# Kernel optimization log

Hardware: AMD Instinct MI355X
Metric: run time of the kernel (lower is better)

## Reference

```python
import jax, jax.numpy as jnp
import numpy as np

NEG_INF = -1e30  # stand-in for -inf in additive causal mask (softmax-safe)


def rotary_pos_emb(x):
    # x: [B, T, H, D]. Faithful to source: freqs = 1/1000**(arange(0,D,2)//D)
    # with INTEGER floor division -> exponent 0 -> all freqs == 1.0.
    B, T, H, D = x.shape
    exponents = (jnp.arange(0, D, 2)[: D // 2] // D).astype(jnp.float32)
    freqs = 1.0 / jnp.power(jnp.float32(1000.0), exponents)          # [D/2]
    theta = jnp.arange(T, dtype=jnp.float32)[:, None] * freqs[None, :]  # [T, D/2]
    cos = jnp.cos(theta)[None, :, None, :]  # [1, T, 1, D/2]
    sin = jnp.sin(theta)[None, :, None, :]
    xr = x.astype(jnp.float32).reshape(B, T, H, D // 2, 2)
    x0, x1 = xr[..., 0], xr[..., 1]
    # complex multiply (x0 + i x1) * (cos + i sin)
    out = jnp.stack([x0 * cos - x1 * sin, x0 * sin + x1 * cos], axis=-1)
    return out.reshape(B, T, H, D).astype(x.dtype)


def attention_fwd(x, wq, wk, wv, wo, n_heads=32):
    B, T, C = x.shape
    hd = C // n_heads  # head_dim = 128
    # nn.Linear(bias=False): y = x @ W^T with W: [out, in]
    xq = (x @ wq.T).reshape(B, T, n_heads, hd)
    xk = (x @ wk.T).reshape(B, T, n_heads, hd)
    xv = (x @ wv.T).reshape(B, T, n_heads, hd)
    xq = rotary_pos_emb(xq)
    xk = rotary_pos_emb(xk)
    # n_rep == 1 -> repeat_kv is identity
    scale = hd ** -0.5
    scores = jnp.einsum('bqhd,bkhd->bhqk', xq, xk) * scale  # [B,H,T,T]
    causal = jnp.tril(jnp.ones((T, T), dtype=bool))
    scores = jnp.where(causal[None, None], scores, NEG_INF)
    probs = jax.nn.softmax(scores.astype(jnp.float32), axis=-1).astype(xq.dtype)
    out = jnp.einsum('bhqk,bkhd->bqhd', probs, xv).reshape(B, T, C)
    return out @ wo.T


def setup_inputs() -> dict:
    key = jax.random.key(0)
    ks = jax.random.split(key, 5)
    B, T, C = 2, 2048, 4096
    s = 0.02
    return {
        'x': jax.random.normal(ks[0], (B, T, C), jnp.float32),
        'wq': jax.random.normal(ks[1], (C, C), jnp.float32) * s,
        'wk': jax.random.normal(ks[2], (C, C), jnp.float32) * s,
        'wv': jax.random.normal(ks[3], (C, C), jnp.float32) * s,
        'wo': jax.random.normal(ks[4], (C, C), jnp.float32) * s,
    }


def reference(x, wq, wk, wv, wo):
    return attention_fwd(x, wq, wk, wv, wo)
```

## Files before the change

### kernel.cpp

```cpp
#include <hip/hip_runtime.h>
#include <hip/hip_bf16.h>
#include <stdint.h>

typedef __bf16 bf16_t;
typedef __attribute__((ext_vector_type(8))) __bf16 bf16x8;
typedef __attribute__((ext_vector_type(4))) float f32x4;

#define GLL16(gptr, lptr)                                                      \
  __builtin_amdgcn_global_load_lds(                                            \
      (__attribute__((address_space(1))) void*)(gptr),                         \
      (__attribute__((address_space(3))) void*)(lptr), 16, 0, 0)

__global__ __launch_bounds__(256) void cast5_kernel(const float* __restrict__ x,
                                                    const float* __restrict__ wq,
                                                    const float* __restrict__ wk,
                                                    const float* __restrict__ wv,
                                                    const float* __restrict__ wo,
                                                    bf16_t* __restrict__ outbase) {
  const size_t SZ = (size_t)4096 * 4096;
  const float* in;
  switch (blockIdx.y) {
    case 0: in = x; break;
    case 1: in = wq; break;
    case 2: in = wk; break;
    case 3: in = wv; break;
    default: in = wo; break;
  }
  bf16_t* out = outbase + (size_t)blockIdx.y * SZ;
  int i = blockIdx.x * 256 + threadIdx.x;
  const float4* p = (const float4*)in + (size_t)i * 2;
  float4 a = p[0], b = p[1];
  bf16x8 o;
  o[0] = (__bf16)a.x; o[1] = (__bf16)a.y; o[2] = (__bf16)a.z; o[3] = (__bf16)a.w;
  o[4] = (__bf16)b.x; o[5] = (__bf16)b.y; o[6] = (__bf16)b.z; o[7] = (__bf16)b.w;
  *((bf16x8*)out + i) = o;
}

#define STAGE_HALF(gbase, ldsbase)                                             \
  do {                                                                         \
    GLL16((gbase) + (size_t)(w * 32 + sr) * 4096 + sq, (ldsbase) + w * 1024);  \
    GLL16((gbase) + (size_t)(w * 32 + 16 + sr) * 4096 + sq,                    \
          (ldsbase) + w * 1024 + 512);                                         \
  } while (0)

#define HALF(buf_, kk_, S1_, S2_, TAIL_)                                       \
  do {                                                                         \
    bf16x8 af0_[4], af1_[4];                                                   \
    _Pragma("unroll") for (int ni = 0; ni < 4; ++ni) bfr[ni] =                 \
        *(const bf16x8*)&Bs[buf_][kk_][(wc * 64 + ni * 16 + l15) * 32 + sl8];  \
    _Pragma("unroll") for (int mi = 0; mi < 4; ++mi) af0_[mi] =                \
        *(const bf16x8*)&As[buf_][kk_][(wr * 128 + mi * 16 + l15) * 32 + sl8]; \
    S1_;                                                                       \
    __builtin_amdgcn_sched_barrier(0);                                         \
    _Pragma("unroll") for (int mi = 0; mi < 4; ++mi) af1_[mi] =                \
        *(const bf16x8*)&As[buf_][kk_][(wr * 128 + 64 + mi * 16 + l15) * 32 +  \
                                       sl8];                                   \
    asm volatile("s_waitcnt lgkmcnt(4)" ::: "memory");                         \
    __builtin_amdgcn_sched_barrier(0);                                         \
    __builtin_amdgcn_s_setprio(1);                                             \
    _Pragma("unroll") for (int mi = 0; mi < 4; ++mi)                           \
        _Pragma("unroll") for (int ni = 0; ni < 4; ++ni)                       \
            acc[mi][ni] = __builtin_amdgcn_mfma_f32_16x16x32_bf16(             \
                af0_[mi], bfr[ni], acc[mi][ni], 0, 0, 0);                      \
    __builtin_amdgcn_s_setprio(0);                                             \
    S2_;                                                                       \
    asm volatile("s_waitcnt lgkmcnt(0)" ::: "memory");                         \
    __builtin_amdgcn_sched_barrier(0);                                         \
    __builtin_amdgcn_s_setprio(1);                                             \
    _Pragma("unroll") for (int mi = 0; mi < 4; ++mi)                           \
        _Pragma("unroll") for (int ni = 0; ni < 4; ++ni)                       \
            acc[4 + mi][ni] = __builtin_amdgcn_mfma_f32_16x16x32_bf16(         \
                af1_[mi], bfr[ni], acc[4 + mi][ni], 0, 0, 0);                  \
    __builtin_amdgcn_s_setprio(0);                                             \
    TAIL_;                                                                     \
    __builtin_amdgcn_s_barrier();                                              \
  } while (0)

#define GEMM256_MAIN(Aptr, Bptr)                                               \
  const bf16_t* Ag = (Aptr) + (size_t)bm * 4096;                               \
  const bf16_t* Bg = (Bptr) + (size_t)bn * 4096;                               \
  f32x4 acc[8][4] = {};                                                        \
  bf16x8 bfr[4];                                                               \
  STAGE_HALF(Ag, &As[0][0][0]);                                                \
  STAGE_HALF(Bg, &Bs[0][0][0]);                                                \
  STAGE_HALF(Ag + 32, &As[0][1][0]);                                           \
  STAGE_HALF(Bg + 32, &Bs[0][1][0]);                                           \
  STAGE_HALF(Ag + 64, &As[1][0][0]);                                           \
  STAGE_HALF(Bg + 64, &Bs[1][0][0]);                                           \
  asm volatile("s_waitcnt vmcnt(4)" ::: "memory");                             \
  __builtin_amdgcn_s_barrier();                                                \
  for (int it = 0; it < 32; ++it) {                                            \
    const int kt = it * 2;                                                     \
    const bool more = (it < 31);                                               \
                                                    \
    HALF(0, 0,                                                                 \
         STAGE_HALF(Ag + (size_t)(kt + 1) * 64 + 32, &As[1][1][0]),            \
         STAGE_HALF(Bg + (size_t)(kt + 1) * 64 + 32, &Bs[1][1][0]), (void)0);  \
    HALF(0, 1,                                                                 \
         if (more) STAGE_HALF(Ag + (size_t)(kt + 2) * 64, &As[0][0][0]),       \
         if (more) STAGE_HALF(Bg + (size_t)(kt + 2) * 64, &Bs[0][0][0]),       \
         if (more) { asm volatile("s_waitcnt vmcnt(4)" ::: "memory"); } else { \
           asm volatile("s_waitcnt vmcnt(0)" ::: "memory"); });                \
                                                  \
    HALF(1, 0,                                                                 \
         if (more) STAGE_HALF(Ag + (size_t)(kt + 2) * 64 + 32, &As[0][1][0]),  \
         if (more) STAGE_HALF(Bg + (size_t)(kt + 2) * 64 + 32, &Bs[0][1][0]),  \
         (void)0);                                                             \
    HALF(1, 1,                                                                 \
         if (more) STAGE_HALF(Ag + (size_t)(kt + 3) * 64, &As[1][0][0]),       \
         if (more) STAGE_HALF(Bg + (size_t)(kt + 3) * 64, &Bs[1][0][0]),       \
         if (more) { asm volatile("s_waitcnt vmcnt(4)" ::: "memory"); });      \
  }

__device__ __forceinline__ void epi_rope256(const f32x4 (&acc)[8][4],
                                            bf16_t* __restrict__ C, int bm,
                                            int bn, int wr, int wc, int quad,
                                            int l15) {
#pragma unroll
  for (int a = 0; a < 8; ++a) {
    const int row0 = bm + wr * 128 + a * 16 + quad * 4;
    float fsv[4], fcv[4];
#pragma unroll
    for (int r = 0; r < 4; ++r)
      sincosf((float)((row0 + r) & 2047), &fsv[r], &fcv[r]);
#pragma unroll
    for (int ni = 0; ni < 4; ++ni) {
      const int col = bn + wc * 64 + ni * 16 + l15;
      const bool odd = (col & 1);
#pragma unroll
      for (int r = 0; r < 4; ++r) {
        float v = acc[a][ni][r];
        float pr = __shfl_xor(v, 1, 64);
        float o = odd ? (pr * fsv[r] + v * fcv[r]) : (v * fcv[r] - pr * fsv[r]);
        C[(size_t)(row0 + r) * 4096 + col] = (__bf16)o;
      }
    }
  }
}

__device__ __forceinline__ void epi_vt256(const f32x4 (&acc)[8][4],
                                          bf16_t* __restrict__ VT, int bm,
                                          int bn, int wr, int wc, int quad,
                                          int l15) {
#pragma unroll
  for (int a = 0; a < 8; ++a) {
    const int row0 = bm + wr * 128 + a * 16 + quad * 4;
    const int b = row0 >> 11, t0 = row0 & 2047;
#pragma unroll
    for (int ni = 0; ni < 4; ++ni) {
      const int col = bn + wc * 64 + ni * 16 + l15;
      const int h = col >> 7, d = col & 127;
      union { __bf16 e[4]; uint2 u; } pk;
#pragma unroll
      for (int r = 0; r < 4; ++r) pk.e[r] = (__bf16)acc[a][ni][r];
      *(uint2*)&VT[((size_t)((b * 32 + h) * 128 + d)) * 2048 + t0] = pk.u;
    }
  }
}

__global__ __launch_bounds__(512, 2) void gemm_qkv(const bf16_t* __restrict__ X,
                                                   const bf16_t* __restrict__ WQ,
                                                   const bf16_t* __restrict__ WK,
                                                   const bf16_t* __restrict__ WV,
                                                   bf16_t* __restrict__ Qo,
                                                   bf16_t* __restrict__ Ko,
                                                   bf16_t* __restrict__ VTo) {
  __shared__ bf16_t As[2][2][8192];
  __shared__ bf16_t Bs[2][2][8192];
  const int tid = threadIdx.x;
  const int w = tid >> 6;
  const int lane = tid & 63;
  const int quad = lane >> 4;
  const int l15 = lane & 15;
  const int wr = w >> 2, wc = w & 3;
  const int sr = lane >> 2;
  const int sq = (((lane & 3) ^ ((lane >> 3) & 3))) * 8;
  const int sl8 = (quad ^ ((l15 >> 1) & 3)) * 8;
  const int mat = blockIdx.y;
  int id = blockIdx.x;
  id = (id & 7) * 32 + (id >> 3);
  const int bm = (id >> 4) * 256, bn = (id & 15) * 256;
  const bf16_t* Bp = (mat == 0) ? WQ : (mat == 1) ? WK : WV;

  GEMM256_MAIN(X, Bp)

  if (mat == 0)
    epi_rope256(acc, Qo, bm, bn, wr, wc, quad, l15);
  else if (mat == 1)
    epi_rope256(acc, Ko, bm, bn, wr, wc, quad, l15);
  else
    epi_vt256(acc, VTo, bm, bn, wr, wc, quad, l15);
}

__global__ __launch_bounds__(512, 2) void gemm_out(const bf16_t* __restrict__ A,
                                                   const bf16_t* __restrict__ B,
                                                   float* __restrict__ C) {
  __shared__ bf16_t As[2][2][8192];
  __shared__ bf16_t Bs[2][2][8192];
  const int tid = threadIdx.x;
  const int w = tid >> 6;
  const int lane = tid & 63;
  const int quad = lane >> 4;
  const int l15 = lane & 15;
  const int wr = w >> 2, wc = w & 3;
  const int sr = lane >> 2;
  const int sq = (((lane & 3) ^ ((lane >> 3) & 3))) * 8;
  const int sl8 = (quad ^ ((l15 >> 1) & 3)) * 8;
  int id = blockIdx.x;
  id = (id & 7) * 32 + (id >> 3);
  const int bm = (id >> 4) * 256, bn = (id & 15) * 256;

  GEMM256_MAIN(A, B)

#pragma unroll
  for (int a = 0; a < 8; ++a) {
    const int row0 = bm + wr * 128 + a * 16 + quad * 4;
#pragma unroll
    for (int ni = 0; ni < 4; ++ni) {
      const int col = bn + wc * 64 + ni * 16 + l15;
#pragma unroll
      for (int r = 0; r < 4; ++r)
        C[(size_t)(row0 + r) * 4096 + col] = acc[a][ni][r];
    }
  }
}

__global__ __launch_bounds__(256) void attn_kernel(const bf16_t* __restrict__ Q,
                                                   const bf16_t* __restrict__ Km,
                                                   const bf16_t* __restrict__ VT,
                                                   bf16_t* __restrict__ O) {
  __shared__ bf16_t Ks[64 * 128];
  __shared__ bf16_t Vts[128 * 64];
  __shared__ bf16_t QPs[64 * 128];
  const int tid = threadIdx.x;
  const int w = tid >> 6;
  const int lane = tid & 63;
  const int quad = lane >> 4;
  const int l15 = lane & 15;
  const int bh = blockIdx.x;
  const int qtile = 31 - blockIdx.y;
  const int mrow_base = (bh >> 5) * 2048;
  const int h = bh & 31;
  const float scale = 0.08838834764831845f;

#pragma unroll
  for (int it = 0; it < 4; ++it) {
    int c = w * 4 + it;
    int row = c * 4 + (lane >> 4);
    int cc = (lane & 15) ^ (row & 15);
    GLL16(Q + (size_t)(mrow_base + qtile * 64 + row) * 4096 + h * 128 + cc * 8,
          &QPs[c * 512]);
  }
  __syncthreads();
  bf16x8 qf[4];
#pragma unroll
  for (int ks = 0; ks < 4; ++ks) {
    int row = w * 16 + l15;
    int slot = (ks * 4 + quad) ^ (row & 15);
    qf[ks] = *(const bf16x8*)&QPs[row * 128 + slot * 8];
  }
  bf16_t* Pw = &QPs[w * 16 * 72];

  f32x4 accO[8] = {};
  float mrun[4], lrun[4];
#pragma unroll
  for (int r = 0; r < 4; ++r) { mrun[r] = -1e30f; lrun[r] = 0.f; }

  for (int kt = 0; kt <= qtile; ++kt) {
    __syncthreads();
#pragma unroll
    for (int it = 0; it < 4; ++it) {
      int c = w * 4 + it;
      int krow = c * 4 + (lane >> 4);
      int kcc = (lane & 15) ^ (krow & 15);
      GLL16(Km + (size_t)(mrow_base + kt * 64 + krow) * 4096 + h * 128 + kcc * 8,
            &Ks[c * 512]);
      int vrow = c * 8 + (lane >> 3);
      int vcc = (lane & 7) ^ (vrow & 7);
      GLL16(VT + (size_t)(bh * 128 + vrow) * 2048 + kt * 64 + vcc * 8,
            &Vts[c * 512]);
    }
    __syncthreads();

    f32x4 s[4];
#pragma unroll
    for (int ni = 0; ni < 4; ++ni) {
      s[ni] = (f32x4){0.f, 0.f, 0.f, 0.f};
#pragma unroll
      for (int ks = 0; ks < 4; ++ks) {
        int row = ni * 16 + l15;
        int slot = (ks * 4 + quad) ^ (row & 15);
        bf16x8 kf = *(const bf16x8*)&Ks[row * 128 + slot * 8];
        s[ni] = __builtin_amdgcn_mfma_f32_16x16x32_bf16(qf[ks], kf, s[ni], 0, 0, 0);
      }
    }
    const bool diag = (kt == qtile);
#pragma unroll
    for (int ni = 0; ni < 4; ++ni)
#pragma unroll
      for (int r = 0; r < 4; ++r) {
        float v = s[ni][r] * scale;
        if (diag && (ni * 16 + l15) > (w * 16 + quad * 4 + r)) v = -1e30f;
        s[ni][r] = v;
      }
    float mx[4], alpha[4], rs[4];
#pragma unroll
    for (int r = 0; r < 4; ++r)
      mx[r] = fmaxf(fmaxf(s[0][r], s[1][r]), fmaxf(s[2][r], s[3][r]));
#pragma unroll
    for (int off = 1; off < 16; off <<= 1)
#pragma unroll
      for (int r = 0; r < 4; ++r) mx[r] = fmaxf(mx[r], __shfl_xor(mx[r], off, 64));
    float ps[4][4];
#pragma unroll
    for (int r = 0; r < 4; ++r) {
      float mn = fmaxf(mrun[r], mx[r]);
      alpha[r] = __expf(mrun[r] - mn);
      mrun[r] = mn;
      rs[r] = 0.f;
    }
#pragma unroll
    for (int ni = 0; ni < 4; ++ni)
#pragma unroll
      for (int r = 0; r < 4; ++r) {
        float p = __expf(s[ni][r] - mrun[r]);
        ps[ni][r] = p;
        rs[r] += p;
      }
#pragma unroll
    for (int off = 1; off < 16; off <<= 1)
#pragma unroll
      for (int r = 0; r < 4; ++r) rs[r] += __shfl_xor(rs[r], off, 64);
#pragma unroll
    for (int r = 0; r < 4; ++r) lrun[r] = lrun[r] * alpha[r] + rs[r];
#pragma unroll
    for (int nt = 0; nt < 8; ++nt)
#pragma unroll
      for (int r = 0; r < 4; ++r) accO[nt][r] *= alpha[r];
#pragma unroll
    for (int ni = 0; ni < 4; ++ni)
#pragma unroll
      for (int r = 0; r < 4; ++r)
        Pw[(quad * 4 + r) * 72 + ni * 16 + l15] = (__bf16)ps[ni][r];
    asm volatile("s_waitcnt lgkmcnt(0)" ::: "memory");
    bf16x8 pf[2];
#pragma unroll
    for (int ks = 0; ks < 2; ++ks)
      pf[ks] = *(const bf16x8*)&Pw[l15 * 72 + ks * 32 + quad * 8];
#pragma unroll
    for (int nt = 0; nt < 8; ++nt)
#pragma unroll
      for (int ks = 0; ks < 2; ++ks) {
        int vrow = nt * 16 + l15;
        int slot = (ks * 4 + quad) ^ (vrow & 7);
        bf16x8 vf = *(const bf16x8*)&Vts[vrow * 64 + slot * 8];
        accO[nt] = __builtin_amdgcn_mfma_f32_16x16x32_bf16(pf[ks], vf, accO[nt], 0, 0, 0);
      }
  }

#pragma unroll
  for (int r = 0; r < 4; ++r) lrun[r] = 1.f / lrun[r];
#pragma unroll
  for (int nt = 0; nt < 8; ++nt)
#pragma unroll
    for (int r = 0; r < 4; ++r) {
      int trow = qtile * 64 + w * 16 + quad * 4 + r;
      int d = nt * 16 + l15;
      O[(size_t)(mrow_base + trow) * 4096 + h * 128 + d] =
          (__bf16)(accO[nt][r] * lrun[r]);
    }
}

extern "C" void kernel_launch(void* const* d_in, const int* in_sizes, int n_in,
                              void* d_out, int out_size, void* d_ws, size_t ws_size,
                              hipStream_t stream) {
  (void)in_sizes; (void)n_in; (void)out_size; (void)ws_size;
  const float* x = (const float*)d_in[0];
  const float* wq = (const float*)d_in[1];
  const float* wk = (const float*)d_in[2];
  const float* wv = (const float*)d_in[3];
  const float* wo = (const float*)d_in[4];
  float* out = (float*)d_out;

  const size_t SZ = (size_t)4096 * 4096;
  bf16_t* xb = (bf16_t*)d_ws;
  bf16_t* wqb = xb + SZ;
  bf16_t* wkb = wqb + SZ;
  bf16_t* wvb = wkb + SZ;
  bf16_t* wob = wvb + SZ;
  bf16_t* qb = wob + SZ;
  bf16_t* kb = qb + SZ;
  bf16_t* vtb = kb + SZ;
  bf16_t* ab = vtb + SZ;

  dim3 b256(256), b512(512);
  cast5_kernel<<<dim3((unsigned)(SZ / 8 / 256), 5), b256, 0, stream>>>(
      x, wq, wk, wv, wo, xb);

  gemm_qkv<<<dim3(256, 3), b512, 0, stream>>>(xb, wqb, wkb, wvb, qb, kb, vtb);

  attn_kernel<<<dim3(64, 32), b256, 0, stream>>>(qb, kb, vtb, ab);

  gemm_out<<<dim3(256), b512, 0, stream>>>(ab, wob, out);
}
```

Baseline: 1.009 ms.

## Double-buffer K/V tiles in attention kernel to overlap loads with MFMA

Splits the attention kernel's K and V shared-memory tiles into two buffers. The next key tile is prefetched with global_load_lds while the current one is being computed, so global-memory latency overlaps with the MFMA and softmax work. The two __syncthreads per iteration become one vmcnt wait plus one barrier, and sched_barriers pin the instruction order. The cost is more LDS per block (K/V storage doubles), which may reduce how many blocks fit on each CU.

Measured after the change: 970.5 us. 3.8% less time.

```diff
diff --git a/kernel.cpp b/kernel.cpp
--- a/kernel.cpp
+++ b/kernel.cpp
@@ -229,8 +229,8 @@
                                                    const bf16_t* __restrict__ Km,
                                                    const bf16_t* __restrict__ VT,
                                                    bf16_t* __restrict__ O) {
-  __shared__ bf16_t Ks[64 * 128];
-  __shared__ bf16_t Vts[128 * 64];
+  __shared__ bf16_t Ks[2][64 * 128];
+  __shared__ bf16_t Vts[2][128 * 64];
   __shared__ bf16_t QPs[64 * 128];
   const int tid = threadIdx.x;
   const int w = tid >> 6;
@@ -243,6 +243,20 @@
   const int h = bh & 31;
   const float scale = 0.08838834764831845f;
 
+#define STAGE_KV(BUF_, KT_)                                                    \
+  _Pragma("unroll") for (int it = 0; it < 4; ++it) {                           \
+    int c = w * 4 + it;                                                        \
+    int krow = c * 4 + (lane >> 4);                                            \
+    int kcc = (lane & 15) ^ (krow & 15);                                       \
+    GLL16(Km + (size_t)(mrow_base + (KT_)*64 + krow) * 4096 + h * 128 +        \
+              kcc * 8,                                                         \
+          &Ks[BUF_][c * 512]);                                                 \
+    int vrow = c * 8 + (lane >> 3);                                            \
+    int vcc = (lane & 7) ^ (vrow & 7);                                         \
+    GLL16(VT + (size_t)(bh * 128 + vrow) * 2048 + (KT_)*64 + vcc * 8,          \
+          &Vts[BUF_][c * 512]);                                                \
+  }
+
 #pragma unroll
   for (int it = 0; it < 4; ++it) {
     int c = w * 4 + it;
@@ -251,7 +265,9 @@
     GLL16(Q + (size_t)(mrow_base + qtile * 64 + row) * 4096 + h * 128 + cc * 8,
           &QPs[c * 512]);
   }
-  __syncthreads();
+  STAGE_KV(0, 0);
+  asm volatile("s_waitcnt vmcnt(8)" ::: "memory");
+  __builtin_amdgcn_sched_barrier(0);
   bf16x8 qf[4];
 #pragma unroll
   for (int ks = 0; ks < 4; ++ks) {
@@ -259,6 +275,8 @@
     int slot = (ks * 4 + quad) ^ (row & 15);
     qf[ks] = *(const bf16x8*)&QPs[row * 128 + slot * 8];
   }
+  asm volatile("s_waitcnt lgkmcnt(0)" ::: "memory");
+  __builtin_amdgcn_sched_barrier(0);
   bf16_t* Pw = &QPs[w * 16 * 72];
 
   f32x4 accO[8] = {};
@@ -267,20 +285,12 @@
   for (int r = 0; r < 4; ++r) { mrun[r] = -1e30f; lrun[r] = 0.f; }
 
   for (int kt = 0; kt <= qtile; ++kt) {
-    __syncthreads();
-#pragma unroll
-    for (int it = 0; it < 4; ++it) {
-      int c = w * 4 + it;
-      int krow = c * 4 + (lane >> 4);
-      int kcc = (lane & 15) ^ (krow & 15);
-      GLL16(Km + (size_t)(mrow_base + kt * 64 + krow) * 4096 + h * 128 + kcc * 8,
-            &Ks[c * 512]);
-      int vrow = c * 8 + (lane >> 3);
-      int vcc = (lane & 7) ^ (vrow & 7);
-      GLL16(VT + (size_t)(bh * 128 + vrow) * 2048 + kt * 64 + vcc * 8,
-            &Vts[c * 512]);
-    }
-    __syncthreads();
+    const int cur = kt & 1;
+    asm volatile("s_waitcnt vmcnt(0)" ::: "memory");
+    __builtin_amdgcn_sched_barrier(0);
+    __builtin_amdgcn_s_barrier();
+    if (kt < qtile) { STAGE_KV(cur ^ 1, kt + 1); }
+    __builtin_amdgcn_sched_barrier(0);
 
     f32x4 s[4];
 #pragma unroll
@@ -290,7 +300,7 @@
       for (int ks = 0; ks < 4; ++ks) {
         int row = ni * 16 + l15;
         int slot = (ks * 4 + quad) ^ (row & 15);
-        bf16x8 kf = *(const bf16x8*)&Ks[row * 128 + slot * 8];
+        bf16x8 kf = *(const bf16x8*)&Ks[cur][row * 128 + slot * 8];
         s[ni] = __builtin_amdgcn_mfma_f32_16x16x32_bf16(qf[ks], kf, s[ni], 0, 0, 0);
       }
     }
@@ -343,6 +353,7 @@
       for (int r = 0; r < 4; ++r)
         Pw[(quad * 4 + r) * 72 + ni * 16 + l15] = (__bf16)ps[ni][r];
     asm volatile("s_waitcnt lgkmcnt(0)" ::: "memory");
+    __builtin_amdgcn_sched_barrier(0);
     bf16x8 pf[2];
 #pragma unroll
     for (int ks = 0; ks < 2; ++ks)
@@ -353,7 +364,7 @@
       for (int ks = 0; ks < 2; ++ks) {
         int vrow = nt * 16 + l15;
         int slot = (ks * 4 + quad) ^ (vrow & 7);
-        bf16x8 vf = *(const bf16x8*)&Vts[vrow * 64 + slot * 8];
+        bf16x8 vf = *(const bf16x8*)&Vts[cur][vrow * 64 + slot * 8];
         accO[nt] = __builtin_amdgcn_mfma_f32_16x16x32_bf16(pf[ks], vf, accO[nt], 0, 0, 0);
       }
   }
@@ -369,6 +380,7 @@
       O[(size_t)(mrow_base + trow) * 4096 + h * 128 + d] =
           (__bf16)(accO[nt][r] * lrun[r]);
     }
+#undef STAGE_KV
 }
 
 extern "C" void kernel_launch(void* const* d_in, const int* in_sizes, int n_in,
```
